# Optimization experiments

Hardware: AMD Instinct MI355X
Metric: run time of the kernel (lower is better)

The kernel has to match this reference:

```python
import jax, jax.numpy as jnp
import numpy as np

N_RADIAL = 8
N_PSEUDO = 4          # Alchemical pseudo-species
EMB_DIM = N_RADIAL * N_PSEUDO  # 32
CUTOFF = 5.0
WIDTH = 0.5
SQRT3_4PI = float(np.sqrt(3.0 / (4.0 * np.pi)))


def _cg_111():
    # Real Clebsch-Gordan coefficients for l1=l2=1 -> L=1.
    # In the real spherical-harmonic ordering (-1,0,1) = (y,z,x) this is the
    # Levi-Civita tensor (permuted), scaled by 1/sqrt(2).
    eps = np.zeros((3, 3, 3), dtype=np.float32)
    for i, j, k in [(0, 1, 2), (1, 2, 0), (2, 0, 1)]:
        eps[i, j, k] = 1.0
        eps[i, k, j] = -1.0
    perm = np.array([1, 2, 0])  # (m=-1,0,1) -> cartesian (y,z,x)
    C = eps[np.ix_(perm, perm, perm)] / np.sqrt(2.0)
    return jnp.asarray(C, dtype=jnp.float32)


def _shifted_cosine(r):
    # ShiftedCosine cutoff function: 1 below rc-w, smooth cosine in [rc-w, rc], 0 above.
    t = (r - (CUTOFF - WIDTH)) / WIDTH
    f = 0.5 * (1.0 + jnp.cos(jnp.pi * jnp.clip(t, 0.0, 1.0)))
    return jnp.where(r < CUTOFF, f, 0.0)


def _radial_basis(r):
    # Laplacian-eigenstate-like radial functions: spherical-Bessel-type sin modes.
    # r: (E,) -> (E, N_RADIAL)
    n = jnp.arange(1, N_RADIAL + 1, dtype=jnp.float32)  # (N_RADIAL,)
    arg = (jnp.pi / CUTOFF) * r[:, None] * n[None, :]
    return jnp.sin(arg) / (r[:, None] + 1e-10)


def setup_inputs() -> dict:
    key = jax.random.key(0)
    k1, k2, k3, k4, k5, k6, k7 = jax.random.split(key, 7)
    E, A, T = 2_000_000, 50_000, 4
    # edge vectors within the cutoff sphere (scaled so |v| mostly < CUTOFF)
    vecs = jax.random.normal(k1, (E, 3), dtype=jnp.float32) * 1.8
    centers = jax.random.randint(k2, (E,), 0, A, dtype=jnp.int32)
    neighbors = jax.random.randint(k3, (E,), 0, A, dtype=jnp.int32)
    species = jax.random.randint(k4, (A,), 0, T, dtype=jnp.int32)
    # learned parameters
    W_species = jax.random.normal(k5, (T, N_PSEUDO), dtype=jnp.float32) * 0.5  # alchemical neighbor embedding
    Emb = jax.random.normal(k6, (T, EMB_DIM), dtype=jnp.float32) * 0.5         # center encoding
    Wc = jax.random.normal(k7, (EMB_DIM, 3), dtype=jnp.float32) * 0.2          # contraction to 3 basis vectors
    return {"interatomic_vectors": vecs, "W_species": W_species, "Emb": Emb,
            "Wc": Wc, "centers": centers, "neighbors": neighbors, "species": species}


def reference(interatomic_vectors, W_species, Emb, Wc, centers, neighbors, species):
    A = species.shape[0]
    E = interatomic_vectors.shape[0]
    r = jnp.linalg.norm(interatomic_vectors, axis=-1)            # (E,)
    fcut = _shifted_cosine(r)                                    # (E,)
    R = _radial_basis(r) * fcut[:, None]                         # (E, n)
    # l=1 real spherical harmonics, (m=-1,0,1) = (y,z,x)/r
    Y = SQRT3_4PI * interatomic_vectors[:, (1, 2, 0)] / (r[:, None] + 1e-10)  # (E, 3)
    edge_feat = Y[:, :, None] * R[:, None, :]                    # (E, 3, n)
    # alchemical neighbor weights
    pseudo = W_species[species[neighbors]]                       # (E, q)
    full = jnp.einsum('emn,eq->emnq', edge_feat, pseudo).reshape(E, 3, EMB_DIM)
    # neighbor-sum spherical expansion per center atom
    spex = jax.ops.segment_sum(full, centers, num_segments=A)   # (A, 3, d)
    # center-type encoding
    spex = spex * Emb[species][:, None, :]                       # (A, 3, d)
    # contract radial/chemical channels to 3 basis vectors
    v = jnp.einsum('amd,dk->amk', spex, Wc)                      # (A, 3mu, 3basis)
    C = _cg_111()
    v3 = jnp.einsum('im,in,mnp->ip', v[:, :, 0], v[:, :, 1], C)  # (A, 3)
    basis = jnp.stack([v[:, :, 0], v[:, :, 1], v3], axis=2)      # (A, 3, 3)
    return basis
```

## Files before the change

### kernel.cpp

```cpp
#include <hip/hip_runtime.h>
#include <hip/hip_fp16.h>
#include <math.h>

#define N_RADIAL 8
#define N_PSEUDO 4
#define EMB_DIM 32
#define CUTOFF 5.0f
#define WIDTH 0.5f
#define SQRT3_4PI 0.48860251190291992f
#define INV_SQRT2 0.70710678118654752f
#define PI_F 3.14159265358979323846f

#define SLICE_SHIFT 7
#define SLICE_SZ 128
#define MAX_NSLICE 2048
#define SCAT_EPB 8192
#define SCAT_THREADS 1024
#define SCAT_ITER (SCAT_EPB / SCAT_THREADS)
#define ACC_THREADS 1024

#define Q_INV 8192.0f
#define Q 1.220703125e-4
#define BIAS_ENC 131072.0f
#define ENC_MAX 262143.0f
#define FIELD_MASK 0x3FFFFFFULL

__global__ void init_kernel(const float* __restrict__ W_species,
                            const float* __restrict__ Emb,
                            const float* __restrict__ Wc,
                            float* __restrict__ G,
                            unsigned int* __restrict__ cursor,
                            int nslice, int cap) {
    int i = threadIdx.x;
    if (i < 256) {
        int k  = i & 1;
        int n  = (i >> 1) & 7;
        int tn = (i >> 4) & 3;
        int tc = i >> 6;
        float acc = 0.0f;
        #pragma unroll
        for (int q = 0; q < N_PSEUDO; ++q) {
            int d = n * N_PSEUDO + q;
            acc += W_species[tn * N_PSEUDO + q] * Emb[tc * EMB_DIM + d] * Wc[d * 3 + k];
        }
        G[i] = acc;
    }
    for (int s = i; s < nslice; s += (int)blockDim.x)
        cursor[s] = (unsigned int)(s * cap);
}

__device__ __forceinline__ bool edge_products(float vx, float vy, float vz,
                                              const float* __restrict__ Gp,
                                              float pr[6]) {
    float r = sqrtf(vx * vx + vy * vy + vz * vz);
    if (r >= CUTOFF) return false;

    float rinv = 1.0f / (r + 1e-10f);

    float t = fminf(fmaxf((r - (CUTOFF - WIDTH)) * (1.0f / WIDTH), 0.0f), 1.0f);
    float fcut = 0.5f * (1.0f + __cosf(PI_F * t));

    float theta = (PI_F / CUTOFF) * r;
    float s1 = __sinf(theta);
    float c1 = __cosf(theta);
    float twoc  = 2.0f * c1;
    float sn_m1 = 0.0f;
    float sn    = s1;

    float s0 = 0.0f, s1a = 0.0f;
    #pragma unroll
    for (int n = 0; n < N_RADIAL; ++n) {
        s0  = fmaf(sn, Gp[n * 2 + 0], s0);
        s1a = fmaf(sn, Gp[n * 2 + 1], s1a);
        float nxt = twoc * sn - sn_m1;
        sn_m1 = sn;
        sn = nxt;
    }
    float coef = rinv * fcut;
    s0 *= coef; s1a *= coef;

    float Y0 = SQRT3_4PI * vy * rinv;
    float Y1 = SQRT3_4PI * vz * rinv;
    float Y2 = SQRT3_4PI * vx * rinv;

    pr[0] = Y0 * s0; pr[1] = Y0 * s1a;
    pr[2] = Y1 * s0; pr[3] = Y1 * s1a;
    pr[4] = Y2 * s0; pr[5] = Y2 * s1a;
    return true;
}

__global__ __launch_bounds__(SCAT_THREADS)
void scatter_kernel(const float* __restrict__ vecs,
                    const int*   __restrict__ centers,
                    const int*   __restrict__ neighbors,
                    const int*   __restrict__ species,
                    unsigned int* __restrict__ cursor,
                    unsigned long long* __restrict__ payload,
                    int E, int nslice, int cap) {
    __shared__ unsigned int hist[MAX_NSLICE];
    for (int i = threadIdx.x; i < nslice; i += blockDim.x) hist[i] = 0u;
    __syncthreads();

    int beg = blockIdx.x * SCAT_EPB;
    int end = min(beg + SCAT_EPB, E);

    unsigned long long word[SCAT_ITER];
    int sl[SCAT_ITER];

    #pragma unroll
    for (int k = 0; k < SCAT_ITER; ++k) {
        sl[k] = -1;
        word[k] = 0;
        int e = beg + k * SCAT_THREADS + (int)threadIdx.x;
        if (e < end) {
            float vx = vecs[3 * e + 0], vy = vecs[3 * e + 1], vz = vecs[3 * e + 2];
            float r2 = vx * vx + vy * vy + vz * vz;
            if (r2 < CUTOFF * CUTOFF) {
                int c = centers[e];
                unsigned int tc = (unsigned int)species[c];
                unsigned int tn = (unsigned int)species[neighbors[e]];
                unsigned int meta = (unsigned int)(c & (SLICE_SZ - 1)) | (tc << 7) | (tn << 9);
                unsigned int hx = (unsigned int)__half_as_ushort(__float2half(vx));
                unsigned int hy = (unsigned int)__half_as_ushort(__float2half(vy));
                unsigned int hz = (unsigned int)__half_as_ushort(__float2half(vz));
                unsigned int lo = hx | (hy << 16);
                unsigned int hi = hz | (meta << 16);
                word[k] = ((unsigned long long)hi << 32) | lo;
                sl[k] = c >> SLICE_SHIFT;
                atomicAdd(&hist[sl[k]], 1u);
            }
        }
    }
    __syncthreads();

    for (int s = threadIdx.x; s < nslice; s += (int)blockDim.x) {
        unsigned int c = hist[s];
        hist[s] = c ? atomicAdd(&cursor[s], c) : 0u;
    }
    __syncthreads();

    #pragma unroll
    for (int k = 0; k < SCAT_ITER; ++k) {
        if (sl[k] >= 0) {
            unsigned int pos = atomicAdd(&hist[sl[k]], 1u);
            if (pos < (unsigned int)((sl[k] + 1) * cap))
                payload[pos] = word[k];
        }
    }
}

__global__ __launch_bounds__(ACC_THREADS)
void accum_kernel(const unsigned long long* __restrict__ payload,
                  const unsigned int* __restrict__ cursor,
                  const float* __restrict__ G,
                  float* __restrict__ out, int A, int cap) {
    __shared__ float Gs[256];
    __shared__ unsigned long long acc64[SLICE_SZ * 3];
    int s = blockIdx.x;

    if (threadIdx.x < 256) Gs[threadIdx.x] = G[threadIdx.x];
    for (int i = threadIdx.x; i < SLICE_SZ * 3; i += blockDim.x) acc64[i] = 0ull;
    __syncthreads();

    unsigned int beg = (unsigned int)(s * cap);
    unsigned int end = min(cursor[s], (unsigned int)((s + 1) * cap));
    for (unsigned int i = beg + threadIdx.x; i < end; i += blockDim.x) {
        unsigned long long w = payload[i];
        unsigned int lo = (unsigned int)w;
        unsigned int hi = (unsigned int)(w >> 32);
        float vx = __half2float(__ushort_as_half((unsigned short)(lo & 0xffffu)));
        float vy = __half2float(__ushort_as_half((unsigned short)(lo >> 16)));
        float vz = __half2float(__ushort_as_half((unsigned short)(hi & 0xffffu)));
        unsigned int meta = hi >> 16;
        int lid = (int)(meta & (SLICE_SZ - 1));
        int tc  = (int)((meta >> 7) & 3);
        int tn  = (int)((meta >> 9) & 3);
        const float* Gp = &Gs[((tc * 4 + tn) * 8) * 2];

        float pr[6];
        if (!edge_products(vx, vy, vz, Gp, pr)) continue;

        unsigned long long* ap = &acc64[lid * 3];
        #pragma unroll
        for (int j = 0; j < 3; ++j) {
            float el = fminf(fmaxf(fmaf(pr[2 * j + 0], Q_INV, BIAS_ENC) + 0.5f, 0.0f), ENC_MAX);
            float eh = fminf(fmaxf(fmaf(pr[2 * j + 1], Q_INV, BIAS_ENC) + 0.5f, 0.0f), ENC_MAX);
            unsigned long long wrd = (1ULL << 52)
                                   | ((unsigned long long)(unsigned int)eh << 26)
                                   | (unsigned long long)(unsigned int)el;
            atomicAdd(ap + j, wrd);
        }
    }
    __syncthreads();

    int a = s * SLICE_SZ + (int)threadIdx.x;
    if (threadIdx.x < SLICE_SZ && a < A) {
        const unsigned long long* wv = &acc64[threadIdx.x * 3];
        float v[6];
        #pragma unroll
        for (int j = 0; j < 3; ++j) {
            unsigned long long x = wv[j];
            float n = (float)(unsigned int)(x >> 52);
            v[2 * j + 0] = (float)((double)(x & FIELD_MASK)         * Q) - n * 16.0f;
            v[2 * j + 1] = (float)((double)((x >> 26) & FIELD_MASK) * Q) - n * 16.0f;
        }

        float a0 = v[0], b0 = v[1];
        float a1 = v[2], b1 = v[3];
        float a2 = v[4], b2 = v[5];

        float c0 = (a1 * b2 - a2 * b1) * INV_SQRT2;
        float c1 = (a2 * b0 - a0 * b2) * INV_SQRT2;
        float c2 = (a0 * b1 - a1 * b0) * INV_SQRT2;

        float* o = out + (size_t)a * 9;
        o[0] = a0; o[1] = b0; o[2] = c0;
        o[3] = a1; o[4] = b1; o[5] = c1;
        o[6] = a2; o[7] = b2; o[8] = c2;
    }
}

__global__ void edge_kernel_fb(const float* __restrict__ vecs,
                               const int* __restrict__ centers,
                               const int* __restrict__ neighbors,
                               const int* __restrict__ species,
                               const float* __restrict__ G,
                               unsigned long long* __restrict__ vacc, int E) {
    __shared__ float Gs[256];
    Gs[threadIdx.x] = G[threadIdx.x];
    __syncthreads();

    int e = blockIdx.x * blockDim.x + threadIdx.x;
    if (e >= E) return;

    float vx = vecs[3 * e + 0], vy = vecs[3 * e + 1], vz = vecs[3 * e + 2];
    int c = centers[e];
    int tc = species[c];
    int tn = species[neighbors[e]];
    const float* Gp = &Gs[((tc * 4 + tn) * 8) * 2];

    float pr[6];
    if (!edge_products(vx, vy, vz, Gp, pr)) return;

    unsigned long long* base = vacc + (size_t)c * 4;
    #pragma unroll
    for (int j = 0; j < 3; ++j) {
        float el = fminf(fmaxf(fmaf(pr[2 * j + 0], Q_INV, BIAS_ENC) + 0.5f, 0.0f), ENC_MAX);
        float eh = fminf(fmaxf(fmaf(pr[2 * j + 1], Q_INV, BIAS_ENC) + 0.5f, 0.0f), ENC_MAX);
        unsigned long long w = (1ULL << 52)
                             | ((unsigned long long)(unsigned int)eh << 26)
                             | (unsigned long long)(unsigned int)el;
        atomicAdd(base + j, w);
    }
}

__global__ void finalize_fb(const unsigned long long* __restrict__ vacc,
                            float* __restrict__ out, int A) {
    int a = blockIdx.x * blockDim.x + threadIdx.x;
    if (a >= A) return;

    const unsigned long long* w = vacc + (size_t)a * 4;
    double v[6];
    #pragma unroll
    for (int j = 0; j < 3; ++j) {
        unsigned long long x = w[j];
        double n = (double)(x >> 52);
        v[2 * j + 0] = (double)(x & FIELD_MASK)         * (double)Q - n * 16.0;
        v[2 * j + 1] = (double)((x >> 26) & FIELD_MASK) * (double)Q - n * 16.0;
    }
    float a0 = (float)v[0], b0 = (float)v[1];
    float a1 = (float)v[2], b1 = (float)v[3];
    float a2 = (float)v[4], b2 = (float)v[5];
    float c0 = (a1 * b2 - a2 * b1) * INV_SQRT2;
    float c1 = (a2 * b0 - a0 * b2) * INV_SQRT2;
    float c2 = (a0 * b1 - a1 * b0) * INV_SQRT2;
    float* o = out + (size_t)a * 9;
    o[0] = a0; o[1] = b0; o[2] = c0;
    o[3] = a1; o[4] = b1; o[5] = c1;
    o[6] = a2; o[7] = b2; o[8] = c2;
}

extern "C" void kernel_launch(void* const* d_in, const int* in_sizes, int n_in,
                              void* d_out, int out_size, void* d_ws, size_t ws_size,
                              hipStream_t stream) {
    const float* vecs      = (const float*)d_in[0];
    const float* W_species = (const float*)d_in[1];
    const float* Emb       = (const float*)d_in[2];
    const float* Wc        = (const float*)d_in[3];
    const int*   centers   = (const int*)d_in[4];
    const int*   neighbors = (const int*)d_in[5];
    const int*   species   = (const int*)d_in[6];

    int E = in_sizes[0] / 3;
    int A = in_sizes[6];

    int nslice = (A + SLICE_SZ - 1) / SLICE_SZ;

    double mean = (double)E / (double)nslice;
    int cap = (int)((mean + 8.0 * sqrt(mean) + 63.0) / 64.0) * 64;

    size_t payloadBytes = (size_t)nslice * (size_t)cap * 8;
    size_t metaBytes    = (size_t)(nslice + 256) * sizeof(float) + 256;
    bool sort_path = (nslice <= MAX_NSLICE) && (ws_size >= payloadBytes + metaBytes);

    if (sort_path) {
        unsigned long long* payload = (unsigned long long*)d_ws;
        unsigned int* cursor = (unsigned int*)((char*)d_ws + payloadBytes);
        float*        G      = (float*)(cursor + nslice);

        init_kernel<<<1, 512, 0, stream>>>(W_species, Emb, Wc, G, cursor,
                                           nslice, cap);
        int nbs = (E + SCAT_EPB - 1) / SCAT_EPB;
        scatter_kernel<<<nbs, SCAT_THREADS, 0, stream>>>(
            vecs, centers, neighbors, species, cursor, payload, E, nslice, cap);
        accum_kernel<<<nslice, ACC_THREADS, 0, stream>>>(
            payload, cursor, G, (float*)d_out, A, cap);
    } else {
        unsigned long long* vacc = (unsigned long long*)d_ws;
        float* G = (float*)(vacc + (size_t)A * 4);
        (void)hipMemsetAsync(vacc, 0, (size_t)A * 4 * sizeof(unsigned long long), stream);
        init_kernel<<<1, 512, 0, stream>>>(W_species, Emb, Wc, G,
                                           (unsigned int*)G, 0, 0);
        const int threads = 256;
        edge_kernel_fb<<<(E + threads - 1) / threads, threads, 0, stream>>>(
            vecs, centers, neighbors, species, G, vacc, E);
        finalize_fb<<<(A + threads - 1) / threads, threads, 0, stream>>>(
            vacc, (float*)d_out, A);
    }
}
```

Measured before the change: 51.18 us.

## Pack species into 2-bit LDS table and double slice size

Species ids are packed at 2 bits per atom in the init kernel and staged into LDS inside the scatter kernel. This replaces two dependent random global gathers per edge with shared-memory lookups. The slice size also grows from 128 to 256 atoms, which halves the number of accumulation blocks and histogram bins and puts more edges in each block. The costs are a larger init launch, an extra LDS load per scatter block, and a packed format that only holds species values below 4.

After: 48.74 us. 4.8% less time.

```diff
diff --git a/kernel.cpp b/kernel.cpp
--- a/kernel.cpp
+++ b/kernel.cpp
@@ -11,13 +11,14 @@
 #define INV_SQRT2 0.70710678118654752f
 #define PI_F 3.14159265358979323846f
 
-#define SLICE_SHIFT 7
-#define SLICE_SZ 128
+#define SLICE_SHIFT 8
+#define SLICE_SZ 256
 #define MAX_NSLICE 2048
 #define SCAT_EPB 8192
 #define SCAT_THREADS 1024
 #define SCAT_ITER (SCAT_EPB / SCAT_THREADS)
 #define ACC_THREADS 1024
+#define MAX_SPEC_WORDS 4096
 
 #define Q_INV 8192.0f
 #define Q 1.220703125e-4
@@ -28,25 +29,42 @@
 __global__ void init_kernel(const float* __restrict__ W_species,
                             const float* __restrict__ Emb,
                             const float* __restrict__ Wc,
+                            const int*   __restrict__ species,
                             float* __restrict__ G,
                             unsigned int* __restrict__ cursor,
-                            int nslice, int cap) {
-    int i = threadIdx.x;
-    if (i < 256) {
-        int k  = i & 1;
-        int n  = (i >> 1) & 7;
-        int tn = (i >> 4) & 3;
-        int tc = i >> 6;
-        float acc = 0.0f;
+                            unsigned int* __restrict__ spec_packed,
+                            int A, int nslice, int cap, int words) {
+    int tid = blockIdx.x * blockDim.x + threadIdx.x;
+
+    if (blockIdx.x == 0) {
+        int i = threadIdx.x;
+        if (i < 256) {
+            int k  = i & 1;
+            int n  = (i >> 1) & 7;
+            int tn = (i >> 4) & 3;
+            int tc = i >> 6;
+            float acc = 0.0f;
+            #pragma unroll
+            for (int q = 0; q < N_PSEUDO; ++q) {
+                int d = n * N_PSEUDO + q;
+                acc += W_species[tn * N_PSEUDO + q] * Emb[tc * EMB_DIM + d] * Wc[d * 3 + k];
+            }
+            G[i] = acc;
+        }
+        for (int s = i; s < nslice; s += (int)blockDim.x)
+            cursor[s] = (unsigned int)(s * cap);
+    }
+
+    for (int w = tid; w < words; w += (int)(gridDim.x * blockDim.x)) {
+        unsigned int v = 0;
+        int base = w * 16;
         #pragma unroll
-        for (int q = 0; q < N_PSEUDO; ++q) {
-            int d = n * N_PSEUDO + q;
-            acc += W_species[tn * N_PSEUDO + q] * Emb[tc * EMB_DIM + d] * Wc[d * 3 + k];
-        }
-        G[i] = acc;
-    }
-    for (int s = i; s < nslice; s += (int)blockDim.x)
-        cursor[s] = (unsigned int)(s * cap);
+        for (int j = 0; j < 16; ++j) {
+            int a = base + j;
+            if (a < A) v |= ((unsigned int)species[a] & 3u) << (2 * j);
+        }
+        spec_packed[w] = v;
+    }
 }
 
 __device__ __forceinline__ bool edge_products(float vx, float vy, float vz,
@@ -89,16 +107,23 @@
     return true;
 }
 
+template <bool LDSSPEC>
 __global__ __launch_bounds__(SCAT_THREADS)
 void scatter_kernel(const float* __restrict__ vecs,
                     const int*   __restrict__ centers,
                     const int*   __restrict__ neighbors,
-                    const int*   __restrict__ species,
+                    const unsigned int* __restrict__ spec_packed,
                     unsigned int* __restrict__ cursor,
                     unsigned long long* __restrict__ payload,
-                    int E, int nslice, int cap) {
+                    int E, int nslice, int cap, int words) {
     __shared__ unsigned int hist[MAX_NSLICE];
+    __shared__ unsigned int spec[LDSSPEC ? MAX_SPEC_WORDS : 1];
+
     for (int i = threadIdx.x; i < nslice; i += blockDim.x) hist[i] = 0u;
+    if constexpr (LDSSPEC) {
+        for (int i = threadIdx.x; i < words; i += blockDim.x)
+            spec[i] = spec_packed[i];
+    }
     __syncthreads();
 
     int beg = blockIdx.x * SCAT_EPB;
@@ -116,10 +141,17 @@
             float vx = vecs[3 * e + 0], vy = vecs[3 * e + 1], vz = vecs[3 * e + 2];
             float r2 = vx * vx + vy * vy + vz * vz;
             if (r2 < CUTOFF * CUTOFF) {
-                int c = centers[e];
-                unsigned int tc = (unsigned int)species[c];
-                unsigned int tn = (unsigned int)species[neighbors[e]];
-                unsigned int meta = (unsigned int)(c & (SLICE_SZ - 1)) | (tc << 7) | (tn << 9);
+                int c  = centers[e];
+                int nb = neighbors[e];
+                unsigned int tc, tn;
+                if constexpr (LDSSPEC) {
+                    tc = (spec[c >> 4]  >> ((c & 15) << 1)) & 3u;
+                    tn = (spec[nb >> 4] >> ((nb & 15) << 1)) & 3u;
+                } else {
+                    tc = (spec_packed[c >> 4]  >> ((c & 15) << 1)) & 3u;
+                    tn = (spec_packed[nb >> 4] >> ((nb & 15) << 1)) & 3u;
+                }
+                unsigned int meta = (unsigned int)(c & (SLICE_SZ - 1)) | (tc << 8) | (tn << 10);
                 unsigned int hx = (unsigned int)__half_as_ushort(__float2half(vx));
                 unsigned int hy = (unsigned int)__half_as_ushort(__float2half(vy));
                 unsigned int hz = (unsigned int)__half_as_ushort(__float2half(vz));
@@ -173,8 +205,8 @@
         float vz = __half2float(__ushort_as_half((unsigned short)(hi & 0xffffu)));
         unsigned int meta = hi >> 16;
         int lid = (int)(meta & (SLICE_SZ - 1));
-        int tc  = (int)((meta >> 7) & 3);
-        int tn  = (int)((meta >> 9) & 3);
+        int tc  = (int)((meta >> 8) & 3);
+        int tn  = (int)((meta >> 10) & 3);
         const float* Gp = &Gs[((tc * 4 + tn) * 8) * 2];
 
         float pr[6];
@@ -193,9 +225,10 @@
     }
     __syncthreads();
 
-    int a = s * SLICE_SZ + (int)threadIdx.x;
-    if (threadIdx.x < SLICE_SZ && a < A) {
-        const unsigned long long* wv = &acc64[threadIdx.x * 3];
+    for (int lid = threadIdx.x; lid < SLICE_SZ; lid += (int)blockDim.x) {
+        int a = s * SLICE_SZ + lid;
+        if (a >= A) break;
+        const unsigned long long* wv = &acc64[lid * 3];
         float v[6];
         #pragma unroll
         for (int j = 0; j < 3; ++j) {
@@ -295,32 +328,45 @@
     int A = in_sizes[6];
 
     int nslice = (A + SLICE_SZ - 1) / SLICE_SZ;
+    int words  = (A + 15) / 16;
 
     double mean = (double)E / (double)nslice;
     int cap = (int)((mean + 8.0 * sqrt(mean) + 63.0) / 64.0) * 64;
 
     size_t payloadBytes = (size_t)nslice * (size_t)cap * 8;
-    size_t metaBytes    = (size_t)(nslice + 256) * sizeof(float) + 256;
+    size_t metaBytes    = ((size_t)nslice + 256 + (size_t)words) * 4 + 256;
     bool sort_path = (nslice <= MAX_NSLICE) && (ws_size >= payloadBytes + metaBytes);
 
     if (sort_path) {
         unsigned long long* payload = (unsigned long long*)d_ws;
         unsigned int* cursor = (unsigned int*)((char*)d_ws + payloadBytes);
         float*        G      = (float*)(cursor + nslice);
-
-        init_kernel<<<1, 512, 0, stream>>>(W_species, Emb, Wc, G, cursor,
-                                           nslice, cap);
+        unsigned int* spec_packed = (unsigned int*)(G + 256);
+
+        int nbi = max(1, (words + 1023) / 1024);
+        init_kernel<<<nbi, 1024, 0, stream>>>(W_species, Emb, Wc, species,
+                                              G, cursor, spec_packed,
+                                              A, nslice, cap, words);
         int nbs = (E + SCAT_EPB - 1) / SCAT_EPB;
-        scatter_kernel<<<nbs, SCAT_THREADS, 0, stream>>>(
-            vecs, centers, neighbors, species, cursor, payload, E, nslice, cap);
+        if (words <= MAX_SPEC_WORDS) {
+            scatter_kernel<true><<<nbs, SCAT_THREADS, 0, stream>>>(
+                vecs, centers, neighbors, spec_packed, cursor, payload,
+                E, nslice, cap, words);
+        } else {
+            scatter_kernel<false><<<nbs, SCAT_THREADS, 0, stream>>>(
+                vecs, centers, neighbors, spec_packed, cursor, payload,
+                E, nslice, cap, words);
+        }
         accum_kernel<<<nslice, ACC_THREADS, 0, stream>>>(
             payload, cursor, G, (float*)d_out, A, cap);
     } else {
         unsigned long long* vacc = (unsigned long long*)d_ws;
         float* G = (float*)(vacc + (size_t)A * 4);
+        unsigned int* cursor_dummy = (unsigned int*)(G + 256);
         (void)hipMemsetAsync(vacc, 0, (size_t)A * 4 * sizeof(unsigned long long), stream);
-        init_kernel<<<1, 512, 0, stream>>>(W_species, Emb, Wc, G,
-                                           (unsigned int*)G, 0, 0);
+        init_kernel<<<1, 1024, 0, stream>>>(W_species, Emb, Wc, species,
+                                            G, cursor_dummy, cursor_dummy,
+                                            0, 0, 0, 0);
         const int threads = 256;
         edge_kernel_fb<<<(E + threads - 1) / threads, threads, 0, stream>>>(
             vecs, centers, neighbors, species, G, vacc, E);
```
